# Optimization experiments

Hardware: AMD Instinct MI355X
Metric: run time of the kernel (lower is better)

The kernel has to match this reference:

```python
import jax, jax.numpy as jnp
import numpy as np

STRIDE = (2, 2)  # from init_kwargs


def setup_inputs() -> dict:
    key = jax.random.key(0)
    kx, kw_, kb = jax.random.split(key, 3)
    x = jax.random.normal(kx, (8, 256, 64, 64), dtype=jnp.float32)
    weight = jax.random.normal(kw_, (128, 256, 4, 4), dtype=jnp.float32) * 0.02
    bias = jax.random.normal(kb, (128, 4, 4), dtype=jnp.float32) * 0.01
    return {"x": x, "weight": weight, "bias": bias}


def reference(x, weight, bias):
    # x: (b, i, h, w); weight: (o, i, kh, kw); bias: (o, kh, kw)
    b, c, h, w = x.shape
    o, _, kh, kw = weight.shape
    sh, sw = STRIDE
    # Outer-product contraction: (b, o, kh, kw, h, w)
    y = jnp.einsum('bihw,oixy->boxyhw', x, weight)
    # Bias is added per kernel position BEFORE the overlap-add fold,
    # so overlapping output pixels accumulate multiple bias copies
    # (faithful to the original module).
    y = y + bias[None, :, :, :, None, None]
    nh = (h - 1) * sh + kh
    nw = (w - 1) * sw + kw
    out = jnp.zeros((b, o, nh, nw), dtype=x.dtype)
    # fold: overlap-add scatter over the kh*kw kernel positions (small fixed loop)
    for ky in range(kh):
        for kxp in range(kw):
            out = out.at[:, :,
                         ky:ky + (h - 1) * sh + 1:sh,
                         kxp:kxp + (w - 1) * sw + 1:sw].add(y[:, :, ky, kxp])
    return out
```

## Files before the change

### kernel.cpp

```cpp
#include <hip/hip_runtime.h>
#include <stdint.h>
#include <stddef.h>

#define GLOBAL_AS __attribute__((address_space(1)))
#define LDS_AS    __attribute__((address_space(3)))

typedef __bf16 bf16x8 __attribute__((ext_vector_type(8)));
typedef float  f32x4  __attribute__((ext_vector_type(4)));

constexpr int NB = 8, CI = 256, H_ = 64, W_ = 64, CO = 128;
constexpr int OH = 130, OW = 130;
constexpr int PU = 65;
constexpr int PAD = 66;

constexpr size_t XPAD_ELEMS = (size_t)NB * PAD * PAD * CI;
constexpr size_t XPAD_BYTES = XPAD_ELEMS * 2;
constexpr size_t SLACK      = 256 * 1024;
constexpr size_t WT_OFF     = XPAD_BYTES + SLACK;
constexpr size_t WT_ELEMS   = (size_t)16 * CO * CI;

__device__ __forceinline__ void gload_lds16(const void* g, void* l) {
  __builtin_amdgcn_global_load_lds((GLOBAL_AS void*)g, (LDS_AS void*)l, 16, 0, 0);
}

__global__ void prep_x(const float* __restrict__ x, __bf16* __restrict__ xp) {
  __shared__ float tile[64][65];
  const int ib = blockIdx.x;
  const int h  = blockIdx.y;
  const int bat = blockIdx.z;
  const int t  = threadIdx.x;
  const int i0 = ib * 64;
  const float* src = x + (((size_t)(bat * CI + i0)) * H_ + h) * W_;
#pragma unroll
  for (int p = 0; p < 16; ++p) {
    int ii = p * 4 + (t >> 6);
    int ww = t & 63;
    tile[ii][ww] = src[(size_t)ii * H_ * W_ + ww];
  }
  __syncthreads();
  __bf16* dst = xp + ((size_t)(bat * PAD + h + 1) * PAD + 1) * CI + i0;
#pragma unroll
  for (int p = 0; p < 16; ++p) {
    int ww = p * 4 + (t >> 6);
    int il = t & 63;
    dst[(size_t)ww * CI + il] = (__bf16)tile[il][ww];
  }
}

__global__ void prep_w(const float* __restrict__ w, __bf16* __restrict__ wt) {
  int tid = blockIdx.x * 256 + threadIdx.x;
  int i   = tid & 255;
  int o   = (tid >> 8) & 127;
  int tap = tid >> 15;
  wt[tid] = (__bf16)w[(size_t)(o * CI + i) * 16 + tap];
}

__global__ __launch_bounds__(256) void deconv_mfma(
    const __bf16* __restrict__ xp, const __bf16* __restrict__ wt,
    const float* __restrict__ bias, float* __restrict__ out) {
  const int wg  = blockIdx.x;
  const int vt  = wg % 5;
  const int ut  = (wg / 5) % 9;
  const int bat = (wg / 45) % 8;
  const int pid = wg / 360;
  const int py = pid >> 1, px = pid & 1;
  const int u0 = ut * 8, v0 = vt * 16;

  __shared__ alignas(16) __bf16 lds[2][8192];

  const int t    = threadIdx.x;
  const int wid  = t >> 6, lane = t & 63;
  const int lr   = lane & 15, kg = lane >> 4;
  const int wr   = wid >> 1, wc = wid & 1;

  const int kst = (t & 3) ^ ((t >> 3) & 3);
  const int m0  = t >> 2;
  const int du0 = m0 >> 4, dv0 = m0 & 15;

  const __bf16* srcA0 = wt + (size_t)m0 * CI + (size_t)kst * 8;
  const __bf16* srcB00 = xp + ((size_t)(bat * PAD + u0 + 1) * PAD + (v0 + 1)) * CI
                         + (size_t)du0 * PAD * CI + (size_t)dv0 * CI + (size_t)kst * 8;

  __bf16* ldsA0[2] = { &lds[0][0] + wid * 512, &lds[1][0] + wid * 512 };
  __bf16* ldsB0[2] = { &lds[0][4096] + wid * 512, &lds[1][4096] + wid * 512 };

  const int swz = (lr >> 1) & 3;
  int offA[4], offB[4];
#pragma unroll
  for (int mt = 0; mt < 4; ++mt) {
    int m = wr * 64 + mt * 16 + lr;
    offA[mt] = m * 32 + ((kg ^ swz) * 8);
  }
#pragma unroll
  for (int nt = 0; nt < 4; ++nt) {
    int n = wc * 64 + nt * 16 + lr;
    offB[nt] = n * 32 + ((kg ^ swz) * 8);
  }

  f32x4 acc[4][4] = {};

  auto stage = [&](int buf, int s) {
    const int tap = s >> 3;
    const int ic  = (s & 7) * 32;
    const int a = tap >> 1, c = tap & 1;
    const int tapW = (py + 2 * a) * 4 + (px + 2 * c);
    const __bf16* sa = srcA0 + (size_t)tapW * CO * CI + ic;
    const __bf16* sb = srcB00 - (size_t)(a * PAD + c) * CI + ic;
    gload_lds16(sa,                          ldsA0[buf]);
    gload_lds16(sa + (size_t)64 * CI,        ldsA0[buf] + 2048);
    gload_lds16(sb,                          ldsB0[buf]);
    gload_lds16(sb + (size_t)4 * PAD * CI,   ldsB0[buf] + 2048);
  };

  stage(0, 0);
  __syncthreads();
  int cur = 0;
  for (int s = 0; s < 32; ++s) {
    if (s < 31) stage(cur ^ 1, s + 1);
    const __bf16* ab = &lds[cur][0];
    const __bf16* bb = &lds[cur][4096];
    bf16x8 af[4], bfr[4];
#pragma unroll
    for (int mt = 0; mt < 4; ++mt) af[mt]  = *(const bf16x8*)(ab + offA[mt]);
#pragma unroll
    for (int nt = 0; nt < 4; ++nt) bfr[nt] = *(const bf16x8*)(bb + offB[nt]);
#pragma unroll
    for (int mt = 0; mt < 4; ++mt)
#pragma unroll
      for (int nt = 0; nt < 4; ++nt)
        acc[mt][nt] = __builtin_amdgcn_mfma_f32_16x16x32_bf16(af[mt], bfr[nt], acc[mt][nt], 0, 0, 0);
    __syncthreads();
    cur ^= 1;
  }

  const int dv = lr, v = v0 + dv;
  const bool vok = (v < PU);
  const bool c0 = (v <= 63), c1 = (v >= 1);
  const int ox = 2 * v + px;
#pragma unroll
  for (int mt = 0; mt < 4; ++mt) {
#pragma unroll
    for (int r = 0; r < 4; ++r) {
      const int o = wr * 64 + mt * 16 + kg * 4 + r;
      const float* bp = bias + (size_t)o * 16;
      const float b00 = bp[py * 4 + px];
      const float b01 = bp[py * 4 + px + 2];
      const float b10 = bp[(py + 2) * 4 + px];
      const float b11 = bp[(py + 2) * 4 + px + 2];
      const size_t orow = (size_t)(bat * CO + o) * (OH * OW);
#pragma unroll
      for (int nt = 0; nt < 4; ++nt) {
        const int du = wc * 4 + nt;
        const int u = u0 + du;
        if (u < PU && vok) {
          const bool a0 = (u <= 63), a1 = (u >= 1);
          float bs = (a0 && c0 ? b00 : 0.f) + (a0 && c1 ? b01 : 0.f)
                   + (a1 && c0 ? b10 : 0.f) + (a1 && c1 ? b11 : 0.f);
          const int oy = 2 * u + py;
          out[orow + (size_t)oy * OW + ox] = acc[mt][nt][r] + bs;
        }
      }
    }
  }
}

extern "C" void kernel_launch(void* const* d_in, const int* in_sizes, int n_in,
                              void* d_out, int out_size, void* d_ws, size_t ws_size,
                              hipStream_t stream) {
  const float* x    = (const float*)d_in[0];
  const float* w    = (const float*)d_in[1];
  const float* bias = (const float*)d_in[2];
  float* out = (float*)d_out;
  char* ws = (char*)d_ws;
  __bf16* xpad = (__bf16*)ws;
  __bf16* wt   = (__bf16*)(ws + WT_OFF);

  hipMemsetAsync(ws, 0, WT_OFF, stream);
  prep_x<<<dim3(4, 64, 8), 256, 0, stream>>>(x, xpad);
  prep_w<<<dim3(2048), 256, 0, stream>>>(w, wt);
  deconv_mfma<<<dim3(1440), 256, 0, stream>>>(xpad, wt, bias, out);
}
```

Before: 176.9 us.

## Fold column parity into GEMM M dimension and flatten pixel tiles

```diff
diff --git a/kernel.cpp b/kernel.cpp
--- a/kernel.cpp
+++ b/kernel.cpp
@@ -12,12 +12,12 @@
 constexpr int OH = 130, OW = 130;
 constexpr int PU = 65;
 constexpr int PAD = 66;
+constexpr int NPIX = PU * PU;
+constexpr int NTILES = 34;
 
 constexpr size_t XPAD_ELEMS = (size_t)NB * PAD * PAD * CI;
 constexpr size_t XPAD_BYTES = XPAD_ELEMS * 2;
-constexpr size_t SLACK      = 256 * 1024;
-constexpr size_t WT_OFF     = XPAD_BYTES + SLACK;
-constexpr size_t WT_ELEMS   = (size_t)16 * CO * CI;
+constexpr size_t WT_OFF     = XPAD_BYTES;
 
 __device__ __forceinline__ void gload_lds16(const void* g, void* l) {
   __builtin_amdgcn_global_load_lds((GLOBAL_AS void*)g, (LDS_AS void*)l, 16, 0, 0);
@@ -25,91 +25,91 @@
 
 __global__ void prep_x(const float* __restrict__ x, __bf16* __restrict__ xp) {
   __shared__ float tile[64][65];
-  const int ib = blockIdx.x;
-  const int h  = blockIdx.y;
-  const int bat = blockIdx.z;
-  const int t  = threadIdx.x;
-  const int i0 = ib * 64;
-  const float* src = x + (((size_t)(bat * CI + i0)) * H_ + h) * W_;
+  const int h   = blockIdx.x;
+  const int bat = blockIdx.y;
+  const int t   = threadIdx.x;
+  for (int ch = 0; ch < 4; ++ch) {
+    const int i0 = ch * 64;
+    const float* src = x + (((size_t)(bat * CI + i0)) * H_ + h) * W_;
+    if (ch) __syncthreads();
 #pragma unroll
-  for (int p = 0; p < 16; ++p) {
-    int ii = p * 4 + (t >> 6);
-    int ww = t & 63;
-    tile[ii][ww] = src[(size_t)ii * H_ * W_ + ww];
-  }
-  __syncthreads();
-  __bf16* dst = xp + ((size_t)(bat * PAD + h + 1) * PAD + 1) * CI + i0;
+    for (int r = 0; r < 4; ++r) {
+      int ii = r * 16 + (t >> 4);
+      int ww = (t & 15) * 4;
+      float4 v = *(const float4*)(src + (size_t)ii * H_ * W_ + ww);
+      tile[ii][ww] = v.x; tile[ii][ww + 1] = v.y; tile[ii][ww + 2] = v.z; tile[ii][ww + 3] = v.w;
+    }
+    __syncthreads();
+    __bf16* dst = xp + ((size_t)(bat * PAD + h + 1) * PAD + 1) * CI + i0;
 #pragma unroll
-  for (int p = 0; p < 16; ++p) {
-    int ww = p * 4 + (t >> 6);
-    int il = t & 63;
-    dst[(size_t)ww * CI + il] = (__bf16)tile[il][ww];
+    for (int r = 0; r < 2; ++r) {
+      int s  = r * 256 + t;
+      int ww = s >> 3;
+      int ig = (s & 7) * 8;
+      bf16x8 o;
+#pragma unroll
+      for (int k = 0; k < 8; ++k) o[k] = (__bf16)tile[ig + k][ww];
+      *(bf16x8*)(dst + (size_t)ww * CI + ig) = o;
+    }
   }
 }
 
-__global__ void prep_w(const float* __restrict__ w, __bf16* __restrict__ wt) {
+__global__ void prep_w2(const float* __restrict__ w, __bf16* __restrict__ wt2) {
   int tid = blockIdx.x * 256 + threadIdx.x;
   int i   = tid & 255;
-  int o   = (tid >> 8) & 127;
-  int tap = tid >> 15;
-  wt[tid] = (__bf16)w[(size_t)(o * CI + i) * 16 + tap];
+  int tap = (tid >> 8) & 3;
+  int row = (tid >> 10) & 255;
+  int py  = tid >> 18;
+  int a = tap >> 1, c = tap & 1;
+  int o = row >> 1, px = row & 1;
+  wt2[tid] = (__bf16)w[(size_t)(o * CI + i) * 16 + (py + 2 * a) * 4 + (px + 2 * c)];
 }
 
-__global__ __launch_bounds__(256) void deconv_mfma(
-    const __bf16* __restrict__ xp, const __bf16* __restrict__ wt,
+__global__ __launch_bounds__(512) void deconv_mfma(
+    const __bf16* __restrict__ xp, const __bf16* __restrict__ wt2,
     const float* __restrict__ bias, float* __restrict__ out) {
-  const int wg  = blockIdx.x;
-  const int vt  = wg % 5;
-  const int ut  = (wg / 5) % 9;
-  const int bat = (wg / 45) % 8;
-  const int pid = wg / 360;
-  const int py = pid >> 1, px = pid & 1;
-  const int u0 = ut * 8, v0 = vt * 16;
+  const int wg    = blockIdx.x;
+  const int nt_i  = wg % NTILES;
+  const int bat   = (wg / NTILES) % 8;
+  const int py    = wg / (NTILES * 8);
+  const int nBase = nt_i * 128;
 
-  __shared__ alignas(16) __bf16 lds[2][8192];
+  __shared__ alignas(16) __bf16 lds[2][12288];
 
   const int t    = threadIdx.x;
   const int wid  = t >> 6, lane = t & 63;
   const int lr   = lane & 15, kg = lane >> 4;
   const int wr   = wid >> 1, wc = wid & 1;
 
-  const int kst = (t & 3) ^ ((t >> 3) & 3);
-  const int m0  = t >> 2;
-  const int du0 = m0 >> 4, dv0 = m0 & 15;
+  const int mA   = t >> 2;
+  const int kstA = (t & 3) ^ ((mA >> 1) & 3);
+  const __bf16* srcA = wt2 + ((size_t)py * 256 + mA) * 1024 + kstA * 8;
 
-  const __bf16* srcA0 = wt + (size_t)m0 * CI + (size_t)kst * 8;
-  const __bf16* srcB00 = xp + ((size_t)(bat * PAD + u0 + 1) * PAD + (v0 + 1)) * CI
-                         + (size_t)du0 * PAD * CI + (size_t)dv0 * CI + (size_t)kst * 8;
-
-  __bf16* ldsA0[2] = { &lds[0][0] + wid * 512, &lds[1][0] + wid * 512 };
-  __bf16* ldsB0[2] = { &lds[0][4096] + wid * 512, &lds[1][4096] + wid * 512 };
+  int pix = nBase + mA;
+  if (pix > NPIX - 1) pix = NPIX - 1;
+  const int uB = pix / PU, vB = pix % PU;
+  const __bf16* srcB = xp + ((size_t)(bat * PAD + uB + 1) * PAD + (vB + 1)) * CI + kstA * 8;
 
   const int swz = (lr >> 1) & 3;
   int offA[4], offB[4];
 #pragma unroll
-  for (int mt = 0; mt < 4; ++mt) {
-    int m = wr * 64 + mt * 16 + lr;
-    offA[mt] = m * 32 + ((kg ^ swz) * 8);
-  }
+  for (int mt = 0; mt < 4; ++mt)
+    offA[mt] = (wr * 64 + mt * 16 + lr) * 32 + ((kg ^ swz) * 8);
 #pragma unroll
-  for (int nt = 0; nt < 4; ++nt) {
-    int n = wc * 64 + nt * 16 + lr;
-    offB[nt] = n * 32 + ((kg ^ swz) * 8);
-  }
+  for (int nt = 0; nt < 4; ++nt)
+    offB[nt] = 8192 + (wc * 64 + nt * 16 + lr) * 32 + ((kg ^ swz) * 8);
 
   f32x4 acc[4][4] = {};
 
   auto stage = [&](int buf, int s) {
-    const int tap = s >> 3;
-    const int ic  = (s & 7) * 32;
-    const int a = tap >> 1, c = tap & 1;
-    const int tapW = (py + 2 * a) * 4 + (px + 2 * c);
-    const __bf16* sa = srcA0 + (size_t)tapW * CO * CI + ic;
-    const __bf16* sb = srcB00 - (size_t)(a * PAD + c) * CI + ic;
-    gload_lds16(sa,                          ldsA0[buf]);
-    gload_lds16(sa + (size_t)64 * CI,        ldsA0[buf] + 2048);
-    gload_lds16(sb,                          ldsB0[buf]);
-    gload_lds16(sb + (size_t)4 * PAD * CI,   ldsB0[buf] + 2048);
+    const int ic = (s & 7) * 32;
+    const int a  = s >> 4, c = (s >> 3) & 1;
+    const __bf16* sa = srcA + s * 32;
+    const __bf16* sb = srcB + ic - (size_t)(a * PAD + c) * CI;
+    __bf16* l = &lds[buf][0];
+    gload_lds16(sa,                    l + (size_t)t * 8);
+    gload_lds16(sa + 128 * 1024,       l + (size_t)t * 8 + 4096);
+    gload_lds16(sb,                    l + 8192 + (size_t)t * 8);
   };
 
   stage(0, 0);
@@ -117,48 +117,51 @@
   int cur = 0;
   for (int s = 0; s < 32; ++s) {
     if (s < 31) stage(cur ^ 1, s + 1);
-    const __bf16* ab = &lds[cur][0];
-    const __bf16* bb = &lds[cur][4096];
-    bf16x8 af[4], bfr[4];
+    const __bf16* base = &lds[cur][0];
+    bf16x8 af[4], bf[4];
 #pragma unroll
-    for (int mt = 0; mt < 4; ++mt) af[mt]  = *(const bf16x8*)(ab + offA[mt]);
+    for (int mt = 0; mt < 4; ++mt) af[mt] = *(const bf16x8*)(base + offA[mt]);
 #pragma unroll
-    for (int nt = 0; nt < 4; ++nt) bfr[nt] = *(const bf16x8*)(bb + offB[nt]);
+    for (int nt = 0; nt < 4; ++nt) bf[nt] = *(const bf16x8*)(base + offB[nt]);
 #pragma unroll
     for (int mt = 0; mt < 4; ++mt)
 #pragma unroll
       for (int nt = 0; nt < 4; ++nt)
-        acc[mt][nt] = __builtin_amdgcn_mfma_f32_16x16x32_bf16(af[mt], bfr[nt], acc[mt][nt], 0, 0, 0);
+        acc[mt][nt] = __builtin_amdgcn_mfma_f32_16x16x32_bf16(af[mt], bf[nt], acc[mt][nt], 0, 0, 0);
     __syncthreads();
     cur ^= 1;
   }
 
-  const int dv = lr, v = v0 + dv;
-  const bool vok = (v < PU);
-  const bool c0 = (v <= 63), c1 = (v >= 1);
-  const int ox = 2 * v + px;
 #pragma unroll
   for (int mt = 0; mt < 4; ++mt) {
+    const int rbase = wr * 64 + mt * 16 + kg * 4;
+    const int o0 = rbase >> 1, o1 = o0 + 1;
 #pragma unroll
-    for (int r = 0; r < 4; ++r) {
-      const int o = wr * 64 + mt * 16 + kg * 4 + r;
-      const float* bp = bias + (size_t)o * 16;
-      const float b00 = bp[py * 4 + px];
-      const float b01 = bp[py * 4 + px + 2];
-      const float b10 = bp[(py + 2) * 4 + px];
-      const float b11 = bp[(py + 2) * 4 + px + 2];
-      const size_t orow = (size_t)(bat * CO + o) * (OH * OW);
-#pragma unroll
-      for (int nt = 0; nt < 4; ++nt) {
-        const int du = wc * 4 + nt;
-        const int u = u0 + du;
-        if (u < PU && vok) {
-          const bool a0 = (u <= 63), a1 = (u >= 1);
-          float bs = (a0 && c0 ? b00 : 0.f) + (a0 && c1 ? b01 : 0.f)
-                   + (a1 && c0 ? b10 : 0.f) + (a1 && c1 ? b11 : 0.f);
-          const int oy = 2 * u + py;
-          out[orow + (size_t)oy * OW + ox] = acc[mt][nt][r] + bs;
-        }
+    for (int nt = 0; nt < 4; ++nt) {
+      const int n = nBase + wc * 64 + nt * 16 + lr;
+      if (n < NPIX) {
+        const int u = n / PU, v = n % PU;
+        const int oy = 2 * u + py;
+        const bool a0 = (u <= 63), a1 = (u >= 1);
+        const bool c0 = (v <= 63), c1 = (v >= 1);
+        auto bs = [&](int o, int px) {
+          const float* bp = bias + (size_t)o * 16;
+          float s0 = 0.f;
+          if (a0 && c0) s0 += bp[py * 4 + px];
+          if (a0 && c1) s0 += bp[py * 4 + px + 2];
+          if (a1 && c0) s0 += bp[(py + 2) * 4 + px];
+          if (a1 && c1) s0 += bp[(py + 2) * 4 + px + 2];
+          return s0;
+        };
+        const size_t b0 = ((size_t)(bat * CO + o0) * OH + oy) * OW + 2 * v;
+        const size_t b1 = ((size_t)(bat * CO + o1) * OH + oy) * OW + 2 * v;
+        float2 w0, w1;
+        w0.x = acc[mt][nt][0] + bs(o0, 0);
+        w0.y = acc[mt][nt][1] + bs(o0, 1);
+        w1.x = acc[mt][nt][2] + bs(o1, 0);
+        w1.y = acc[mt][nt][3] + bs(o1, 1);
+        *(float2*)(out + b0) = w0;
+        *(float2*)(out + b1) = w1;
       }
     }
   }
@@ -173,10 +176,10 @@
   float* out = (float*)d_out;
   char* ws = (char*)d_ws;
   __bf16* xpad = (__bf16*)ws;
-  __bf16* wt   = (__bf16*)(ws + WT_OFF);
+  __bf16* wt2  = (__bf16*)(ws + WT_OFF);
 
-  hipMemsetAsync(ws, 0, WT_OFF, stream);
-  prep_x<<<dim3(4, 64, 8), 256, 0, stream>>>(x, xpad);
-  prep_w<<<dim3(2048), 256, 0, stream>>>(w, wt);
-  deconv_mfma<<<dim3(1440), 256, 0, stream>>>(xpad, wt, bias, out);
+  hipMemsetAsync(xpad, 0, XPAD_BYTES, stream);
+  prep_x<<<dim3(64, 8), 256, 0, stream>>>(x, xpad);
+  prep_w2<<<dim3(2048), 256, 0, stream>>>(w, wt2);
+  deconv_mfma<<<dim3(544), 512, 0, stream>>>(xpad, wt2, bias, out);
 }
```

After: 188.7 us. 6.7% more time.
